# Kernel tuning notes

Hardware: AMD Instinct MI355X
Metric: run time of the kernel (lower is better)

## Reference

```python
import jax, jax.numpy as jnp
import numpy as np

B, N_X, N_A, DIM = 2, 2048, 2048, 1024
HEADS, DH = 16, 64
SEG = 256
ROPE_THETA = 10000.0


def mh_rmsnorm(t, gamma):
    # t: [b,h,n,d], gamma: [h,1,d]; F.normalize(dim=-1) * gamma * sqrt(d)
    norm = jnp.linalg.norm(t, axis=-1, keepdims=True)
    return t / jnp.clip(norm, 1e-12) * gamma * (DH ** 0.5)


def apply_rope(t):
    # t: [b,h,n,d]; GPT-NeoX style half-split rotary over packed positions
    n = t.shape[2]
    half = DH // 2
    inv_freq = ROPE_THETA ** (-jnp.arange(0, half, dtype=jnp.float32) / half)
    freqs = jnp.arange(n, dtype=jnp.float32)[:, None] * inv_freq[None, :]  # [n, half]
    cos, sin = jnp.cos(freqs), jnp.sin(freqs)
    t1, t2 = t[..., :half], t[..., half:]
    return jnp.concatenate([t1 * cos - t2 * sin, t2 * cos + t1 * sin], axis=-1)


def infini_attention(q, k, v, beta):
    # q,k,v: [b,h,n,d]; causal local attention per segment + recurrent linear memory
    b, h, n, d = q.shape
    s = n // SEG
    scale = d ** -0.5
    gate = jax.nn.sigmoid(beta).reshape(1, h, 1, 1)
    causal = jnp.tril(jnp.ones((SEG, SEG), dtype=bool))

    def to_segs(t):  # -> [s, b, h, SEG, d]
        return jnp.moveaxis(t.reshape(b, h, s, SEG, d), 2, 0)

    qs, ks, vs = to_segs(q), to_segs(k), to_segs(v)

    def step(carry, inp):
        M, z = carry  # M: [b,h,d,d], z: [b,h,d]
        q_s, k_s, v_s = inp
        sq = jax.nn.elu(q_s) + 1.0
        sk = jax.nn.elu(k_s) + 1.0
        # memory retrieval
        num = jnp.einsum('bhld,bhde->bhle', sq, M)
        den = jnp.einsum('bhld,bhd->bhl', sq, z)[..., None] + 1e-6
        a_mem = num / den
        # local causal attention within segment
        scores = jnp.einsum('bhid,bhjd->bhij', q_s, k_s) * scale
        scores = jnp.where(causal, scores, -jnp.inf)
        a_loc = jnp.einsum('bhij,bhjd->bhid', jax.nn.softmax(scores, axis=-1), v_s)
        out = gate * a_mem + (1.0 - gate) * a_loc
        # memory update
        M = M + jnp.einsum('bhld,bhle->bhde', sk, v_s)
        z = z + sk.sum(axis=2)
        return (M, z), out

    M0 = jnp.zeros((b, h, d, d), dtype=q.dtype)
    z0 = jnp.zeros((b, h, d), dtype=q.dtype)
    _, outs = jax.lax.scan(step, (M0, z0), (qs, ks, vs))  # [s,b,h,SEG,d]
    return jnp.moveaxis(outs, 0, 2).reshape(b, h, n, d)


def setup_inputs() -> dict:
    key = jax.random.key(0)
    ks = jax.random.split(key, 4)
    scale = DIM ** -0.5
    x = jax.random.normal(ks[0], (B, N_X, DIM), dtype=jnp.float32)
    a = jax.random.normal(ks[1], (B, N_A, DIM), dtype=jnp.float32)
    w_qkv_x = jax.random.normal(ks[2], (DIM, 3 * HEADS * DH), dtype=jnp.float32) * scale
    w_qkv_a = jax.random.normal(ks[3], (DIM, 3 * HEADS * DH), dtype=jnp.float32) * scale
    g = lambda: jnp.ones((HEADS, 1, DH), dtype=jnp.float32)
    beta = jnp.zeros((HEADS,), dtype=jnp.float32)
    return {"x": x, "a": a, "w_qkv_x": w_qkv_x, "w_qkv_a": w_qkv_a,
            "gq_x": g(), "gk_x": g(), "gq_a": g(), "gk_a": g(), "beta": beta}


def _split_heads(t):
    b, n, _ = t.shape
    q, k, v = jnp.split(t, 3, axis=-1)
    r = lambda u: u.reshape(b, n, HEADS, DH).transpose(0, 2, 1, 3)
    return r(q), r(k), r(v)


def reference(x, a, w_qkv_x, w_qkv_a, gq_x, gk_x, gq_a, gk_a, beta):
    q_x, k_x, v_x = _split_heads(x @ w_qkv_x)
    q_a, k_a, v_a = _split_heads(a @ w_qkv_a)
    q_x, k_x = mh_rmsnorm(q_x, gq_x), mh_rmsnorm(k_x, gk_x)
    q_a, k_a = mh_rmsnorm(q_a, gq_a), mh_rmsnorm(k_a, gk_a)
    # pack: a-stream first, then x-stream (matches pack([._a, ._x]))
    q = jnp.concatenate([q_a, q_x], axis=2)
    k = jnp.concatenate([k_a, k_x], axis=2)
    v = jnp.concatenate([v_a, v_x], axis=2)
    q, k = apply_rope(q), apply_rope(k)
    out = infini_attention(q, k, v, beta)  # [b,h,n_a+n_x,d]
    out_a, out_x = out[:, :, :N_A], out[:, :, N_A:]
    merge = lambda t: t.transpose(0, 2, 1, 3).reshape(t.shape[0], t.shape[2], HEADS * DH)
    return merge(out_x), merge(out_a)
```

## Files before the change

### kernel.cpp

```cpp
#include <hip/hip_runtime.h>

#define HEADS 16
#define DH    64
#define NA    2048
#define NX    2048
#define NTOT  4096
#define DIMK  1024
#define NQKV  3072
#define SEG   256
#define NSEG  16

typedef float          f32x4  __attribute__((ext_vector_type(4)));
typedef short          bf16x8 __attribute__((ext_vector_type(8)));
typedef unsigned int   u32x4  __attribute__((ext_vector_type(4)));

__device__ __forceinline__ unsigned short f2bf(float f){
  unsigned int u = __builtin_bit_cast(unsigned int, f);
  unsigned int r = 0x7fffu + ((u >> 16) & 1u);
  return (unsigned short)((u + r) >> 16);
}
__device__ __forceinline__ float bf2f(unsigned short u){
  return __builtin_bit_cast(float, ((unsigned int)u) << 16);
}
__device__ __forceinline__ unsigned pack2(float a, float b){
  return (unsigned)f2bf(a) | ((unsigned)f2bf(b) << 16);
}

__global__ __launch_bounds__(256) void zero_kernel(float* __restrict__ out, int n){
  int i = blockIdx.x * 256 + threadIdx.x;
  if (i < n) out[i] = 0.f;
}

__global__ __launch_bounds__(256) void cvt_kernel(const float* __restrict__ x, const float* __restrict__ a,
                                                  unsigned short* __restrict__ Xb, unsigned short* __restrict__ Ab){
  int i = blockIdx.x * 256 + threadIdx.x;
  const float* src = (i < 1048576) ? x : a;
  unsigned short* dst = (i < 1048576) ? Xb : Ab;
  const int j = i & 1048575;
  float4 v = ((const float4*)src)[j];
  ushort4 o;
  o.x = f2bf(v.x); o.y = f2bf(v.y); o.z = f2bf(v.z); o.w = f2bf(v.w);
  ((ushort4*)dst)[j] = o;
}

__global__ __launch_bounds__(256) void wtr_kernel(const float* __restrict__ Wx, const float* __restrict__ Wa,
                                                  unsigned short* __restrict__ WTx, unsigned short* __restrict__ WTa){
  __shared__ float tile[32][33];
  const float* W = blockIdx.z ? Wa : Wx;
  unsigned short* WT = blockIdx.z ? WTa : WTx;
  int c0 = blockIdx.x * 32, k0 = blockIdx.y * 32;
  int tx = threadIdx.x, ty = threadIdx.y;
  #pragma unroll
  for (int i = 0; i < 32; i += 8) tile[ty+i][tx] = W[(size_t)(k0+ty+i)*NQKV + c0 + tx];
  __syncthreads();
  #pragma unroll
  for (int i = 0; i < 32; i += 8) WT[(size_t)(c0+ty+i)*DIMK + k0 + tx] = f2bf(tile[tx][ty+i]);
}

__global__ __launch_bounds__(256) void rope_tab_kernel(float* __restrict__ tab){
  const int idx = blockIdx.x * 256 + threadIdx.x;
  const int n = idx >> 5, d = idx & 31;
  const float ang = (float)n * expf(-(float)d * 0.28782313662425572f);
  float sn, cs;
  sincosf(ang, &sn, &cs);
  float2 p; p.x = cs; p.y = sn;
  ((float2*)tab)[idx] = p;
}

__global__ __launch_bounds__(256,2) void gemm_qkv_kernel(
    const unsigned short* __restrict__ Xb, const unsigned short* __restrict__ Ab,
    const unsigned short* __restrict__ WTx, const unsigned short* __restrict__ WTa,
    unsigned short* __restrict__ qb, unsigned short* __restrict__ kb,
    unsigned short* __restrict__ vt,
    const float* __restrict__ gqx, const float* __restrict__ gkx,
    const float* __restrict__ gqa, const float* __restrict__ gka,
    const float* __restrict__ tab)
{
  __shared__ __align__(16) unsigned short As0[128*64];
  __shared__ __align__(16) unsigned short Bs0[128*64];
  __shared__ __align__(16) unsigned short As1[128*64];
  __shared__ __align__(16) unsigned short Bs1[128*64];

  const int bid = blockIdx.x;
  const int lid = (bid & 7) * 192 + (bid >> 3);
  const int strm = lid / 768;
  const int rem  = lid - strm * 768;
  const int c0 = (rem >> 5) * 128;
  const int m0 = (rem & 31) * 128;

  const unsigned short* Xp = strm ? Ab  : Xb;
  const unsigned short* Wp = strm ? WTa : WTx;
  const float* gq = strm ? gqa : gqx;
  const float* gk = strm ? gka : gkx;
  const int n_off = strm ? 0 : NA;

  const int tid  = threadIdx.x;
  const int lane = tid & 63, w = tid >> 6;
  const int wr = w >> 1, wc = w & 1;
  const int li = lane & 15, lg = lane >> 4;

  const int sr8  = lane >> 3;
  const int sch  = lane & 7;
  const int sswz = sch ^ sr8;
  const int rsw  = li & 7;

  f32x4 acc[4][4] = {};

  auto stage = [&](unsigned short* AsX, unsigned short* BsX, int kk){
    #pragma unroll
    for (int jj = 0; jj < 4; jj++){
      const int j = w*4 + jj;
      const int r = j*8 + sr8;
      __builtin_amdgcn_global_load_lds(
        (const __attribute__((address_space(1))) unsigned int*)(Xp + (size_t)(m0+r)*DIMK + kk + sswz*8),
        (__attribute__((address_space(3))) unsigned int*)(AsX + j*512), 16, 0, 0);
      __builtin_amdgcn_global_load_lds(
        (const __attribute__((address_space(1))) unsigned int*)(Wp + (size_t)(c0+r)*DIMK + kk + sswz*8),
        (__attribute__((address_space(3))) unsigned int*)(BsX + j*512), 16, 0, 0);
    }
  };
  auto compute = [&](const unsigned short* AsX, const unsigned short* BsX){
    #pragma unroll
    for (int kb2 = 0; kb2 < 2; kb2++){
      bf16x8 af[4], bf[4];
      const int slot = ((kb2*4 + lg) ^ rsw) * 8;
      #pragma unroll
      for (int m = 0; m < 4; m++)
        af[m] = *(const bf16x8*)(&AsX[(wr*64 + m*16 + li)*64 + slot]);
      #pragma unroll
      for (int n = 0; n < 4; n++)
        bf[n] = *(const bf16x8*)(&BsX[(wc*64 + n*16 + li)*64 + slot]);
      #pragma unroll
      for (int m = 0; m < 4; m++)
        #pragma unroll
        for (int n = 0; n < 4; n++)
          acc[m][n] = __builtin_amdgcn_mfma_f32_16x16x32_bf16(af[m], bf[n], acc[m][n], 0, 0, 0);
    }
  };

  stage(As0, Bs0, 0);
  __syncthreads();
  for (int t = 0; t < 16; t += 2){
    stage(As1, Bs1, (t+1)*64);
    compute(As0, Bs0);
    __syncthreads();
    if (t + 2 < 16) stage(As0, Bs0, (t+2)*64);
    compute(As1, Bs1);
    __syncthreads();
  }

  const int colbase = c0 + wc*64;
  const int which = colbase >> 10;
  const int h = (colbase >> 6) & 15;

  if (which < 2){
    const float* gv = (which == 0) ? gq : gk;
    unsigned short* dstb = (which == 0) ? qb : kb;
    float gl[4];
    #pragma unroll
    for (int n = 0; n < 4; n++) gl[n] = gv[h*64 + n*16 + li];
    #pragma unroll
    for (int m = 0; m < 4; m++){
      #pragma unroll
      for (int r = 0; r < 4; r++){
        float ss = acc[m][0][r]*acc[m][0][r] + acc[m][1][r]*acc[m][1][r]
                 + acc[m][2][r]*acc[m][2][r] + acc[m][3][r]*acc[m][3][r];
        ss += __shfl_xor(ss, 1, 64);
        ss += __shfl_xor(ss, 2, 64);
        ss += __shfl_xor(ss, 4, 64);
        ss += __shfl_xor(ss, 8, 64);
        const float sc = 8.0f / fmaxf(sqrtf(ss), 1e-12f);
        float v0 = acc[m][0][r]*sc*gl[0], v1 = acc[m][1][r]*sc*gl[1];
        float v2 = acc[m][2][r]*sc*gl[2], v3 = acc[m][3][r]*sc*gl[3];
        const int row = m0 + wr*64 + m*16 + lg*4 + r;
        const int bb = row >> 11, nn = row & 2047;
        const int n_g = nn + n_off;
        const float2 cs0 = ((const float2*)tab)[n_g*32 + li];
        const float2 cs1 = ((const float2*)tab)[n_g*32 + 16 + li];
        const float o0 = v0*cs0.x - v2*cs0.y;
        const float o1 = v1*cs1.x - v3*cs1.y;
        const float o2 = v2*cs0.x + v0*cs0.y;
        const float o3 = v3*cs1.x + v1*cs1.y;
        unsigned short* drow = dstb + ((size_t)(bb*HEADS + h)*NTOT + (size_t)n_g)*64;
        drow[li]      = f2bf(o0);
        drow[16 + li] = f2bf(o1);
        drow[32 + li] = f2bf(o2);
        drow[48 + li] = f2bf(o3);
      }
    }
  } else {
    #pragma unroll
    for (int m = 0; m < 4; m++){
      #pragma unroll
      for (int r = 0; r < 4; r++){
        const int row = m0 + wr*64 + m*16 + lg*4 + r;
        const int bb = row >> 11, nn = row & 2047;
        const int n_g = nn + n_off;
        unsigned short* vbase = vt + (size_t)(bb*HEADS + h)*DH*NTOT + n_g;
        #pragma unroll
        for (int n = 0; n < 4; n++)
          vbase[(size_t)(n*16 + li)*NTOT] = f2bf(acc[m][n][r]);
      }
    }
  }
}

__global__ __launch_bounds__(256,2) void segG_kernel(const unsigned short* __restrict__ kb,
                                                     const unsigned short* __restrict__ vt,
                                                     float* __restrict__ G, float* __restrict__ zc){
  __shared__ unsigned short skT[64*264];
  __shared__ unsigned short Vts[64*264];
  const int blk = blockIdx.x;
  const int bh = blk >> 4, s = blk & 15;
  const int tid = threadIdx.x;
  const int w = tid >> 6, lane = tid & 63;
  const int li = lane & 15, lg = lane >> 4;
  const size_t segoffb = ((size_t)bh * NTOT + (size_t)s * SEG) * DH;

  #pragma unroll
  for (int it = 0; it < 8; it++){
    const int idx = tid + it*256;
    const int e = idx >> 5, jc = idx & 31;
    *(u32x4*)(Vts + e*264 + jc*8) =
      *(const u32x4*)(vt + (size_t)bh*DH*NTOT + (size_t)e*NTOT + s*SEG + jc*8);
  }
  #pragma unroll
  for (int it = 0; it < 8; it++){
    const int idx = tid + it*256;
    const int l = idx >> 3, dc = idx & 7;
    bf16x8 kk = *(const bf16x8*)(kb + segoffb + (size_t)l*64 + dc*8);
    #pragma unroll
    for (int t2 = 0; t2 < 8; t2++){
      const float xx = bf2f((unsigned short)kk[t2]);
      skT[(dc*8 + t2)*264 + l] = f2bf(xx > 0.f ? xx + 1.f : __expf(xx));
    }
  }
  __syncthreads();

  {
    const int d = tid >> 2, q = tid & 3;
    float zz = 0.f;
    #pragma unroll
    for (int u = 0; u < 8; u++){
      bf16x8 vv = *(const bf16x8*)(skT + d*264 + q*64 + u*8);
      #pragma unroll
      for (int t2 = 0; t2 < 8; t2++)
        zz += bf2f((unsigned short)vv[t2]);
    }
    zz += __shfl_xor(zz, 1, 64);
    zz += __shfl_xor(zz, 2, 64);
    if (q == 0) zc[(size_t)blk*64 + d] = zz;
  }

  f32x4 acc[4] = {};
  #pragma unroll
  for (int k0 = 0; k0 < 256; k0 += 32){
    bf16x8 af = *(const bf16x8*)(skT + (w*16 + li)*264 + k0 + lg*8);
    #pragma unroll
    for (int n = 0; n < 4; n++){
      bf16x8 bf = *(const bf16x8*)(Vts + (n*16 + li)*264 + k0 + lg*8);
      acc[n] = __builtin_amdgcn_mfma_f32_16x16x32_bf16(af, bf, acc[n], 0, 0, 0);
    }
  }
  float* Gout = G + (size_t)blk * DH * DH;
  #pragma unroll
  for (int n = 0; n < 4; n++)
    #pragma unroll
    for (int r = 0; r < 4; r++)
      Gout[(w*16 + lg*4 + r)*64 + n*16 + li] = acc[n][r];
}

__global__ __launch_bounds__(256) void prefix_kernel(const float* __restrict__ G,
                                                     const float* __restrict__ zc,
                                                     float* __restrict__ Mp, float* __restrict__ zp){
  const int bh = blockIdx.x, c = blockIdx.y, tid = threadIdx.x;
  const int e = c*512 + tid;
  float run0 = 0.f, run1 = 0.f;
  for (int s = 0; s < NSEG; s++){
    const size_t base = ((size_t)bh * NSEG + s) * 4096;
    Mp[base + e]       = run0;  run0 += G[base + e];
    Mp[base + e + 256] = run1;  run1 += G[base + e + 256];
  }
  if (c == 0 && tid < DH){
    float rz = 0.f;
    for (int s = 0; s < NSEG; s++){
      zp[((size_t)bh*NSEG + s)*DH + tid] = rz;
      rz += zc[((size_t)bh*NSEG + s)*DH + tid];
    }
  }
}

__global__ __launch_bounds__(256,1) void attn_mfma_kernel(
    const unsigned short* __restrict__ qb, const unsigned short* __restrict__ kb,
    const unsigned short* __restrict__ vt, const float* __restrict__ Mp,
    const float* __restrict__ zp, const float* __restrict__ beta,
    float* __restrict__ out)
{
  __shared__ unsigned short Qs[256*72];
  __shared__ unsigned short KSs[256*72];
  __shared__ unsigned short Vts[64*264];
  __shared__ unsigned short Ps[4*64*72];
  __shared__ unsigned short Mts[64*72];
  __shared__ float den_s[256];
  __shared__ float zsh[64];

  const int blk = blockIdx.x;
  const int s = blk & 15, bh = blk >> 4;
  const int h = bh & 15, b = bh >> 4;
  const int tid = threadIdx.x;
  const int w = tid >> 6, lane = tid & 63;
  const int li = lane & 15, lg = lane >> 4;
  const size_t segoffb = ((size_t)bh * NTOT + (size_t)s * SEG) * DH;

  #pragma unroll
  for (int it = 0; it < 8; it++){
    const int idx = tid + it*256;
    const int row = idx >> 3, jc = idx & 7;
    *(u32x4*)(Qs  + row*72 + jc*8) = *(const u32x4*)(qb + segoffb + (size_t)row*64 + jc*8);
    *(u32x4*)(KSs + row*72 + jc*8) = *(const u32x4*)(kb + segoffb + (size_t)row*64 + jc*8);
  }
  #pragma unroll
  for (int it = 0; it < 8; it++){
    const int idx = tid + it*256;
    const int e = idx >> 5, jc = idx & 31;
    *(u32x4*)(Vts + e*264 + jc*8) =
      *(const u32x4*)(vt + (size_t)bh*DH*NTOT + (size_t)e*NTOT + s*SEG + jc*8);
  }
  #pragma unroll
  for (int it = 0; it < 16; it++){
    const int idx = tid + it*256;
    const int d = idx >> 6, e = idx & 63;
    Mts[e*72 + d] = f2bf(Mp[(size_t)blk*4096 + d*64 + e]);
  }
  if (tid < 64) zsh[tid] = zp[(size_t)blk*64 + tid];
  __syncthreads();

  f32x4 o_acc[4][4] = {};
  float denr[4] = {0.f, 0.f, 0.f, 0.f};
  const int qrow0 = w*64;
  bf16x8 qf[4][2];
  #pragma unroll
  for (int it = 0; it < 4; it++)
    #pragma unroll
    for (int kb2 = 0; kb2 < 2; kb2++)
      qf[it][kb2] = *(const bf16x8*)(Qs + (qrow0 + it*16 + li)*72 + kb2*32 + lg*8);

  for (int c = 0; c <= w; c++){
    f32x4 st[4][4] = {};
    #pragma unroll
    for (int jt = 0; jt < 4; jt++){
      bf16x8 kf0 = *(const bf16x8*)(KSs + (c*64 + jt*16 + li)*72 + 0  + lg*8);
      bf16x8 kf1 = *(const bf16x8*)(KSs + (c*64 + jt*16 + li)*72 + 32 + lg*8);
      #pragma unroll
      for (int it = 0; it < 4; it++){
        st[jt][it] = __builtin_amdgcn_mfma_f32_16x16x32_bf16(kf0, qf[it][0], st[jt][it], 0, 0, 0);
        st[jt][it] = __builtin_amdgcn_mfma_f32_16x16x32_bf16(kf1, qf[it][1], st[jt][it], 0, 0, 0);
      }
    }
    const bool diag = (c == w);
    #pragma unroll
    for (int jt = 0; jt < 4; jt++){
      #pragma unroll
      for (int it = 0; it < 4; it++){
        f32x4 p = st[jt][it];
        unsigned pb[4];
        #pragma unroll
        for (int r = 0; r < 4; r++){
          float pe = __expf(p[r] * 0.125f);
          if (diag && (jt*16 + lg*4 + r > it*16 + li)) pe = 0.f;
          pb[r] = __builtin_bit_cast(unsigned, pe) & 0xFFFF0000u;
          p[r] = __builtin_bit_cast(float, pb[r]);
        }
        denr[it] += (p[0] + p[1]) + (p[2] + p[3]);
        uint2 pkk;
        pkk.x = (pb[0] >> 16) | pb[1];
        pkk.y = (pb[2] >> 16) | pb[3];
        *(uint2*)(Ps + w*4608 + (it*16 + li)*72 + jt*16 + lg*4) = pkk;
      }
    }
    bf16x8 pf[4][2];
    #pragma unroll
    for (int it = 0; it < 4; it++)
      #pragma unroll
      for (int kb2 = 0; kb2 < 2; kb2++)
        pf[it][kb2] = *(const bf16x8*)(Ps + w*4608 + (it*16 + li)*72 + kb2*32 + lg*8);
    #pragma unroll
    for (int et = 0; et < 4; et++){
      bf16x8 vf0 = *(const bf16x8*)(Vts + (et*16 + li)*264 + c*64 + 0  + lg*8);
      bf16x8 vf1 = *(const bf16x8*)(Vts + (et*16 + li)*264 + c*64 + 32 + lg*8);
      #pragma unroll
      for (int it = 0; it < 4; it++){
        o_acc[it][et] = __builtin_amdgcn_mfma_f32_16x16x32_bf16(pf[it][0], vf0, o_acc[it][et], 0, 0, 0);
        o_acc[it][et] = __builtin_amdgcn_mfma_f32_16x16x32_bf16(pf[it][1], vf1, o_acc[it][et], 0, 0, 0);
      }
    }
  }

  #pragma unroll
  for (int it = 0; it < 4; it++){
    denr[it] += __shfl_xor(denr[it], 16, 64);
    denr[it] += __shfl_xor(denr[it], 32, 64);
  }
  if (lane < 16){
    #pragma unroll
    for (int it = 0; it < 4; it++) den_s[qrow0 + it*16 + lane] = denr[it];
  }
  const float gate = 1.f / (1.f + __expf(-beta[h]));
  __syncthreads();

  {
    const int i = tid;
    float sqv[64];
    float denm = 0.f;
    #pragma unroll
    for (int u = 0; u < 8; u++){
      bf16x8 qv = *(const bf16x8*)(Qs + i*72 + u*8);
      #pragma unroll
      for (int t2 = 0; t2 < 8; t2++){
        float x = bf2f((unsigned short)qv[t2]);
        float sq = x > 0.f ? x + 1.f : __expf(x);
        sqv[u*8 + t2] = sq;
        denm += sq * zsh[u*8 + t2];
      }
    }
    const float c2 = gate / (denm + 1e-6f);
    #pragma unroll
    for (int u = 0; u < 16; u++){
      uint2 pw;
      pw.x = pack2(sqv[u*4]*c2,   sqv[u*4+1]*c2);
      pw.y = pack2(sqv[u*4+2]*c2, sqv[u*4+3]*c2);
      *(uint2*)(KSs + i*72 + u*4) = pw;
    }
  }
  __syncthreads();

  #pragma unroll
  for (int it = 0; it < 4; it++){
    #pragma unroll
    for (int r = 0; r < 4; r++){
      const float c1 = (1.f - gate) / den_s[qrow0 + it*16 + lg*4 + r];
      #pragma unroll
      for (int et = 0; et < 4; et++) o_acc[it][et][r] *= c1;
    }
  }
  #pragma unroll
  for (int kb2 = 0; kb2 < 2; kb2++){
    bf16x8 mf[4];
    #pragma unroll
    for (int et = 0; et < 4; et++)
      mf[et] = *(const bf16x8*)(Mts + (et*16 + li)*72 + kb2*32 + lg*8);
    #pragma unroll
    for (int it = 0; it < 4; it++){
      bf16x8 sf = *(const bf16x8*)(KSs + (qrow0 + it*16 + li)*72 + kb2*32 + lg*8);
      #pragma unroll
      for (int et = 0; et < 4; et++)
        o_acc[it][et] = __builtin_amdgcn_mfma_f32_16x16x32_bf16(sf, mf[et], o_acc[it][et], 0, 0, 0);
    }
  }

  #pragma unroll
  for (int it = 0; it < 4; it++){
    #pragma unroll
    for (int r = 0; r < 4; r++){
      const int n_g = s*SEG + qrow0 + it*16 + lg*4 + r;
      size_t o;
      if (n_g >= NA) o = ((size_t)b * NX + (size_t)(n_g - NA)) * 1024 + h * 64;
      else           o = 4194304u + ((size_t)b * NA + (size_t)n_g) * 1024 + h * 64;
      #pragma unroll
      for (int et = 0; et < 4; et++)
        out[o + et*16 + li] = o_acc[it][et][r];
    }
  }
}

extern "C" void kernel_launch(void* const* d_in, const int* in_sizes, int n_in,
                              void* d_out, int out_size, void* d_ws, size_t ws_size,
                              hipStream_t stream)
{
  (void)ws_size;
  const int expect[9] = {4194304, 4194304, 3145728, 3145728, 1024, 1024, 1024, 1024, 16};
  bool ok = (n_in == 9);
  if (ok) for (int i = 0; i < 9; i++) if (in_sizes[i] != expect[i]) { ok = false; break; }
  float* out = (float*)d_out;
  if (!ok){
    zero_kernel<<<dim3((out_size + 255)/256), dim3(256), 0, stream>>>(out, out_size);
    return;
  }

  const float* x    = (const float*)d_in[0];
  const float* a    = (const float*)d_in[1];
  const float* wx   = (const float*)d_in[2];
  const float* wa   = (const float*)d_in[3];
  const float* gqx  = (const float*)d_in[4];
  const float* gkx  = (const float*)d_in[5];
  const float* gqa  = (const float*)d_in[6];
  const float* gka  = (const float*)d_in[7];
  const float* beta = (const float*)d_in[8];

  char* wsb = (char*)d_ws;
  unsigned short* qb  = (unsigned short*)wsb;
  unsigned short* kb  = qb + 8388608;
  unsigned short* vtb = kb + 8388608;
  unsigned short* Xb  = vtb + 8388608;
  unsigned short* Ab  = Xb + 4194304;
  unsigned short* WTx = Ab + 4194304;
  unsigned short* WTa = WTx + 3145728;
  float* ropetab = (float*)(WTa + 3145728);
  float* G   = ropetab + 262144;
  float* Mp  = G + 2097152;
  float* zc  = Mp + 2097152;
  float* zpb = zc + 32768;

  cvt_kernel<<<dim3(8192), dim3(256), 0, stream>>>(x, a, Xb, Ab);
  wtr_kernel<<<dim3(96,32,2), dim3(32,8), 0, stream>>>(wx, wa, WTx, WTa);
  rope_tab_kernel<<<dim3(512), dim3(256), 0, stream>>>(ropetab);
  gemm_qkv_kernel<<<dim3(1536), dim3(256), 0, stream>>>(Xb, Ab, WTx, WTa, qb, kb, vtb,
                                                        gqx, gkx, gqa, gka, ropetab);
  segG_kernel<<<dim3(512), dim3(256), 0, stream>>>(kb, vtb, G, zc);
  prefix_kernel<<<dim3(32,8), dim3(256), 0, stream>>>(G, zc, Mp, zpb);
  attn_mfma_kernel<<<dim3(512), dim3(256), 0, stream>>>(qb, kb, vtb, Mp, zpb, beta, out);
}
```

Measured before the change: 142.3 us.

## Merge prep kernels into one launch and keep attention Q/sq operands in registers

Folds the bf16 conversion, weight transpose and rope-table kernels into a single prep launch that dispatches on block index, removing two kernel launches and the gaps between them. In the attention kernel, Q fragments are now loaded straight from global memory into registers instead of staging through a shared-memory Q tile. The memory-retrieval sq operand is computed from those register fragments, with the row denominator reduced by cross-lane shuffles, and the softmax denominators are read by shuffles rather than a shared array. This frees LDS and drops two block-wide barriers. The cost is more register pressure and uncoalesced 16-byte global loads for Q.

Measured after the change: 135.7 us. 4.6% less time.

```diff
diff --git a/kernel.cpp b/kernel.cpp
--- a/kernel.cpp
+++ b/kernel.cpp
@@ -31,40 +31,45 @@
   if (i < n) out[i] = 0.f;
 }
 
-__global__ __launch_bounds__(256) void cvt_kernel(const float* __restrict__ x, const float* __restrict__ a,
-                                                  unsigned short* __restrict__ Xb, unsigned short* __restrict__ Ab){
-  int i = blockIdx.x * 256 + threadIdx.x;
-  const float* src = (i < 1048576) ? x : a;
-  unsigned short* dst = (i < 1048576) ? Xb : Ab;
-  const int j = i & 1048575;
-  float4 v = ((const float4*)src)[j];
-  ushort4 o;
-  o.x = f2bf(v.x); o.y = f2bf(v.y); o.z = f2bf(v.z); o.w = f2bf(v.w);
-  ((ushort4*)dst)[j] = o;
-}
-
-__global__ __launch_bounds__(256) void wtr_kernel(const float* __restrict__ Wx, const float* __restrict__ Wa,
-                                                  unsigned short* __restrict__ WTx, unsigned short* __restrict__ WTa){
+__global__ __launch_bounds__(256) void prep_kernel(
+    const float* __restrict__ x, const float* __restrict__ a,
+    const float* __restrict__ Wx, const float* __restrict__ Wa,
+    unsigned short* __restrict__ Xb, unsigned short* __restrict__ Ab,
+    unsigned short* __restrict__ WTx, unsigned short* __restrict__ WTa,
+    float* __restrict__ tab)
+{
   __shared__ float tile[32][33];
-  const float* W = blockIdx.z ? Wa : Wx;
-  unsigned short* WT = blockIdx.z ? WTa : WTx;
-  int c0 = blockIdx.x * 32, k0 = blockIdx.y * 32;
-  int tx = threadIdx.x, ty = threadIdx.y;
-  #pragma unroll
-  for (int i = 0; i < 32; i += 8) tile[ty+i][tx] = W[(size_t)(k0+ty+i)*NQKV + c0 + tx];
-  __syncthreads();
-  #pragma unroll
-  for (int i = 0; i < 32; i += 8) WT[(size_t)(c0+ty+i)*DIMK + k0 + tx] = f2bf(tile[tx][ty+i]);
-}
-
-__global__ __launch_bounds__(256) void rope_tab_kernel(float* __restrict__ tab){
-  const int idx = blockIdx.x * 256 + threadIdx.x;
-  const int n = idx >> 5, d = idx & 31;
-  const float ang = (float)n * expf(-(float)d * 0.28782313662425572f);
-  float sn, cs;
-  sincosf(ang, &sn, &cs);
-  float2 p; p.x = cs; p.y = sn;
-  ((float2*)tab)[idx] = p;
+  const int bid = blockIdx.x, tid = threadIdx.x;
+  if (bid < 8192){
+    const int i = bid * 256 + tid;
+    const float* src = (i < 1048576) ? x : a;
+    unsigned short* dst = (i < 1048576) ? Xb : Ab;
+    const int j = i & 1048575;
+    float4 v = ((const float4*)src)[j];
+    ushort4 o;
+    o.x = f2bf(v.x); o.y = f2bf(v.y); o.z = f2bf(v.z); o.w = f2bf(v.w);
+    ((ushort4*)dst)[j] = o;
+  } else if (bid < 14336){
+    const int wid = bid - 8192;
+    const int z = wid / 3072, rem = wid - z*3072;
+    const float* W = z ? Wa : Wx;
+    unsigned short* WT = z ? WTa : WTx;
+    const int c0 = (rem % 96) * 32, k0 = (rem / 96) * 32;
+    const int tx = tid & 31, ty = tid >> 5;
+    #pragma unroll
+    for (int i = 0; i < 32; i += 8) tile[ty+i][tx] = W[(size_t)(k0+ty+i)*NQKV + c0 + tx];
+    __syncthreads();
+    #pragma unroll
+    for (int i = 0; i < 32; i += 8) WT[(size_t)(c0+ty+i)*DIMK + k0 + tx] = f2bf(tile[tx][ty+i]);
+  } else {
+    const int idx = (bid - 14336) * 256 + tid;
+    const int n = idx >> 5, d = idx & 31;
+    const float ang = (float)n * expf(-(float)d * 0.28782313662425572f);
+    float sn, cs;
+    sincosf(ang, &sn, &cs);
+    float2 p; p.x = cs; p.y = sn;
+    ((float2*)tab)[idx] = p;
+  }
 }
 
 __global__ __launch_bounds__(256,2) void gemm_qkv_kernel(
@@ -296,12 +301,10 @@
     const float* __restrict__ zp, const float* __restrict__ beta,
     float* __restrict__ out)
 {
-  __shared__ unsigned short Qs[256*72];
   __shared__ unsigned short KSs[256*72];
   __shared__ unsigned short Vts[64*264];
   __shared__ unsigned short Ps[4*64*72];
   __shared__ unsigned short Mts[64*72];
-  __shared__ float den_s[256];
   __shared__ float zsh[64];
 
   const int blk = blockIdx.x;
@@ -316,7 +319,6 @@
   for (int it = 0; it < 8; it++){
     const int idx = tid + it*256;
     const int row = idx >> 3, jc = idx & 7;
-    *(u32x4*)(Qs  + row*72 + jc*8) = *(const u32x4*)(qb + segoffb + (size_t)row*64 + jc*8);
     *(u32x4*)(KSs + row*72 + jc*8) = *(const u32x4*)(kb + segoffb + (size_t)row*64 + jc*8);
   }
   #pragma unroll
@@ -333,17 +335,18 @@
     Mts[e*72 + d] = f2bf(Mp[(size_t)blk*4096 + d*64 + e]);
   }
   if (tid < 64) zsh[tid] = zp[(size_t)blk*64 + tid];
+
+  const int qrow0 = w*64;
+  bf16x8 qf[4][2];
+  #pragma unroll
+  for (int it = 0; it < 4; it++)
+    #pragma unroll
+    for (int kb2 = 0; kb2 < 2; kb2++)
+      qf[it][kb2] = *(const bf16x8*)(qb + segoffb + (size_t)(qrow0 + it*16 + li)*64 + kb2*32 + lg*8);
   __syncthreads();
 
   f32x4 o_acc[4][4] = {};
   float denr[4] = {0.f, 0.f, 0.f, 0.f};
-  const int qrow0 = w*64;
-  bf16x8 qf[4][2];
-  #pragma unroll
-  for (int it = 0; it < 4; it++)
-    #pragma unroll
-    for (int kb2 = 0; kb2 < 2; kb2++)
-      qf[it][kb2] = *(const bf16x8*)(Qs + (qrow0 + it*16 + li)*72 + kb2*32 + lg*8);
 
   for (int c = 0; c <= w; c++){
     f32x4 st[4][4] = {};
@@ -401,44 +404,41 @@
     denr[it] += __shfl_xor(denr[it], 16, 64);
     denr[it] += __shfl_xor(denr[it], 32, 64);
   }
-  if (lane < 16){
-    #pragma unroll
-    for (int it = 0; it < 4; it++) den_s[qrow0 + it*16 + lane] = denr[it];
-  }
   const float gate = 1.f / (1.f + __expf(-beta[h]));
-  __syncthreads();
-
-  {
-    const int i = tid;
-    float sqv[64];
+
+  bf16x8 sqf[4][2];
+  #pragma unroll
+  for (int it = 0; it < 4; it++){
+    float sqv[16];
     float denm = 0.f;
     #pragma unroll
-    for (int u = 0; u < 8; u++){
-      bf16x8 qv = *(const bf16x8*)(Qs + i*72 + u*8);
+    for (int kb2 = 0; kb2 < 2; kb2++){
       #pragma unroll
       for (int t2 = 0; t2 < 8; t2++){
-        float x = bf2f((unsigned short)qv[t2]);
-        float sq = x > 0.f ? x + 1.f : __expf(x);
-        sqv[u*8 + t2] = sq;
-        denm += sq * zsh[u*8 + t2];
+        const float xq = bf2f((unsigned short)qf[it][kb2][t2]);
+        const float sq = xq > 0.f ? xq + 1.f : __expf(xq);
+        sqv[kb2*8 + t2] = sq;
+        denm += sq * zsh[kb2*32 + lg*8 + t2];
       }
     }
+    denm += __shfl_xor(denm, 16, 64);
+    denm += __shfl_xor(denm, 32, 64);
     const float c2 = gate / (denm + 1e-6f);
     #pragma unroll
-    for (int u = 0; u < 16; u++){
-      uint2 pw;
-      pw.x = pack2(sqv[u*4]*c2,   sqv[u*4+1]*c2);
-      pw.y = pack2(sqv[u*4+2]*c2, sqv[u*4+3]*c2);
-      *(uint2*)(KSs + i*72 + u*4) = pw;
-    }
-  }
-  __syncthreads();
+    for (int kb2 = 0; kb2 < 2; kb2++){
+      union { bf16x8 v; unsigned u[4]; } cc;
+      #pragma unroll
+      for (int p2 = 0; p2 < 4; p2++)
+        cc.u[p2] = pack2(sqv[kb2*8 + 2*p2] * c2, sqv[kb2*8 + 2*p2 + 1] * c2);
+      sqf[it][kb2] = cc.v;
+    }
+  }
 
   #pragma unroll
   for (int it = 0; it < 4; it++){
     #pragma unroll
     for (int r = 0; r < 4; r++){
-      const float c1 = (1.f - gate) / den_s[qrow0 + it*16 + lg*4 + r];
+      const float c1 = (1.f - gate) / __shfl(denr[it], lg*4 + r, 64);
       #pragma unroll
       for (int et = 0; et < 4; et++) o_acc[it][et][r] *= c1;
     }
@@ -451,10 +451,9 @@
       mf[et] = *(const bf16x8*)(Mts + (et*16 + li)*72 + kb2*32 + lg*8);
     #pragma unroll
     for (int it = 0; it < 4; it++){
-      bf16x8 sf = *(const bf16x8*)(KSs + (qrow0 + it*16 + li)*72 + kb2*32 + lg*8);
       #pragma unroll
       for (int et = 0; et < 4; et++)
-        o_acc[it][et] = __builtin_amdgcn_mfma_f32_16x16x32_bf16(sf, mf[et], o_acc[it][et], 0, 0, 0);
+        o_acc[it][et] = __builtin_amdgcn_mfma_f32_16x16x32_bf16(sqf[it][kb2], mf[et], o_acc[it][et], 0, 0, 0);
     }
   }
 
@@ -511,9 +510,7 @@
   float* zc  = Mp + 2097152;
   float* zpb = zc + 32768;
 
-  cvt_kernel<<<dim3(8192), dim3(256), 0, stream>>>(x, a, Xb, Ab);
-  wtr_kernel<<<dim3(96,32,2), dim3(32,8), 0, stream>>>(wx, wa, WTx, WTa);
-  rope_tab_kernel<<<dim3(512), dim3(256), 0, stream>>>(ropetab);
+  prep_kernel<<<dim3(14848), dim3(256), 0, stream>>>(x, a, wx, wa, Xb, Ab, WTx, WTa, ropetab);
   gemm_qkv_kernel<<<dim3(1536), dim3(256), 0, stream>>>(Xb, Ab, WTx, WTa, qb, kb, vtb,
                                                         gqx, gkx, gqa, gka, ropetab);
   segG_kernel<<<dim3(512), dim3(256), 0, stream>>>(kb, vtb, G, zc);
```
